# Optimization experiments

Measured on AMD Instinct MI355X. Metric: run time of the kernel, lower is better.

Reference implementation:

```python
import jax, jax.numpy as jnp
import numpy as np

B, P, D, G, N_IMGS, TEMP = 16, 4096, 512, 64, 5000, 0.01


def bilinear_grid_sample(img, grid):
    """F.grid_sample(img, grid, mode='bilinear', padding_mode='zeros', align_corners=False).
    img: (B, C, H, W); grid: (B, Hg, Wg, 2) with grid[...,0]=x, grid[...,1]=y in [-1,1].
    Returns (B, C, Hg*Wg)."""
    b, c, h, w = img.shape
    gx = grid[..., 0].reshape(b, -1)  # (B, N)
    gy = grid[..., 1].reshape(b, -1)
    # align_corners=False mapping to pixel coords
    ix = ((gx + 1.0) * w - 1.0) * 0.5
    iy = ((gy + 1.0) * h - 1.0) * 0.5
    ix0 = jnp.floor(ix)
    iy0 = jnp.floor(iy)
    ix1 = ix0 + 1.0
    iy1 = iy0 + 1.0
    wx1 = ix - ix0
    wx0 = 1.0 - wx1
    wy1 = iy - iy0
    wy0 = 1.0 - wy1
    flat = img.reshape(b, c, h * w)

    def gather(xi, yi):
        valid = (xi >= 0) & (xi < w) & (yi >= 0) & (yi < h)
        idx = (jnp.clip(yi, 0, h - 1) * w + jnp.clip(xi, 0, w - 1)).astype(jnp.int32)
        vals = jnp.take_along_axis(flat, jnp.broadcast_to(idx[:, None, :], (b, c, idx.shape[-1])), axis=2)
        return vals * valid[:, None, :].astype(img.dtype)

    out = (gather(ix0, iy0) * (wx0 * wy0)[:, None, :]
           + gather(ix1, iy0) * (wx1 * wy0)[:, None, :]
           + gather(ix0, iy1) * (wx0 * wy1)[:, None, :]
           + gather(ix1, iy1) * (wx1 * wy1)[:, None, :])
    return out  # (B, C, N)


def setup_inputs() -> dict:
    key = jax.random.key(0)
    ks = jax.random.split(key, 12)
    sc = 1.0 / np.sqrt(D)
    return {
        "x": jax.random.normal(ks[0], (B, P, D), dtype=jnp.float32),
        "Wq": jax.random.normal(ks[1], (D, D), dtype=jnp.float32) * sc,
        "bq": jnp.zeros((D,), dtype=jnp.float32),
        "Wk": jax.random.normal(ks[2], (D, D), dtype=jnp.float32) * sc,
        "bk": jnp.zeros((D,), dtype=jnp.float32),
        "Wv": jax.random.normal(ks[3], (D, D), dtype=jnp.float32) * sc,
        "bv": jnp.zeros((D,), dtype=jnp.float32),
        "avgs": jnp.zeros((N_IMGS, 2, P), dtype=jnp.float32),
        "std_devs": jnp.ones((N_IMGS, 2, P), dtype=jnp.float32),
        "noise_x": jax.random.normal(ks[4], (B, 1, P), dtype=jnp.float32),
        "noise_y": jax.random.normal(ks[5], (B, 1, P), dtype=jnp.float32),
        "img_ids": jax.random.randint(ks[6], (B,), 0, N_IMGS),
        "mask": jnp.ones((B, P), dtype=bool),
    }


def reference(x, Wq, bq, Wk, bk, Wv, bv, avgs, std_devs, noise_x, noise_y, img_ids, mask):
    b, s, d = x.shape
    q = x @ Wq.T + bq
    k = x @ Wk.T + bk
    v = x @ Wv.T + bv
    a = avgs[img_ids]       # (B, 2, P)
    sd = std_devs[img_ids]  # (B, 2, P)
    sample_x = jnp.tanh((noise_x + a[:, 0:1, :]) * sd[:, 0:1, :])  # (B,1,P)
    sample_y = jnp.tanh((noise_y + a[:, 1:2, :]) * sd[:, 1:2, :])  # (B,1,P)
    grid = jnp.concatenate([sample_x, sample_y], axis=1).reshape(b, G, G, 2)
    k_img = jnp.transpose(k, (0, 2, 1)).reshape(b, d, G, G)
    v_img = jnp.transpose(v, (0, 2, 1)).reshape(b, d, G, G)
    sampled_k = jnp.transpose(bilinear_grid_sample(k_img, grid), (0, 2, 1))  # (B, P, D)
    sampled_v = jnp.transpose(bilinear_grid_sample(v_img, grid), (0, 2, 1))
    scores = jnp.sum(sampled_k * q, axis=-1)  # (B, P)
    attention = jax.nn.sigmoid(TEMP * scores)[..., None] * sampled_v  # (B, P, D)
    return attention
```

## Files before the change

kernel.cpp:

```cpp
#include <hip/hip_runtime.h>
#include <math.h>


typedef __attribute__((ext_vector_type(8))) short s16x8;
typedef __attribute__((ext_vector_type(4))) float f32x4;

__device__ __forceinline__ unsigned short f2bf(float f) {
    unsigned u = __float_as_uint(f);
    u += 0x7FFFu + ((u >> 16) & 1u);
    return (unsigned short)(u >> 16);
}

__device__ __forceinline__ void gload_lds16(const void* g, void* l) {
    __builtin_amdgcn_global_load_lds(
        (const __attribute__((address_space(1))) unsigned int*)g,
        (__attribute__((address_space(3))) unsigned int*)l, 16, 0, 0);
}

__global__ __launch_bounds__(256) void cvt_all(
    const float* __restrict__ x, const float* __restrict__ Wq,
    const float* __restrict__ Wk, const float* __restrict__ Wv,
    unsigned short* __restrict__ xbf, unsigned short* __restrict__ wbf)
{
    const int i = blockIdx.x * 256 + threadIdx.x;
    const float* src;
    unsigned short* dst;
    size_t off;
    if (i < 4194304) {
        src = x; dst = xbf; off = (size_t)i;
    } else {
        int t = i - 4194304;
        int w = t >> 15;
        off = (size_t)(t & 32767);
        src = (w == 0) ? Wq : (w == 1 ? Wk : Wv);
        dst = wbf + (size_t)w * 512 * 512;
    }
    const float4* s = (const float4*)src + 2 * off;
    float4 a = s[0], b = s[1];
    uint4 o;
    o.x = (unsigned)f2bf(a.x) | ((unsigned)f2bf(a.y) << 16);
    o.y = (unsigned)f2bf(a.z) | ((unsigned)f2bf(a.w) << 16);
    o.z = (unsigned)f2bf(b.x) | ((unsigned)f2bf(b.y) << 16);
    o.w = (unsigned)f2bf(b.z) | ((unsigned)f2bf(b.w) << 16);
    ((uint4*)dst)[off] = o;
}

template<int T, int NVM, bool STAGE>
__device__ __forceinline__ void tile_step(
    char* ldsc, const unsigned short* aP, const unsigned short* bP,
    int tid, int abase, int bbase, f32x4 (&acc)[8][4])
{
    asm volatile("s_waitcnt vmcnt(%0)" :: "i"(NVM) : "memory");
    __builtin_amdgcn_s_barrier();
    __builtin_amdgcn_sched_barrier(0);
    const char* lp = ldsc + (T & 3) * 32768;
    s16x8 bfr[4], af[4];
    #pragma unroll
    for (int j = 0; j < 4; ++j) bfr[j] = *(const s16x8*)(lp + bbase + j * 256);
    #pragma unroll
    for (int u = 0; u < 4; ++u) af[u] = *(const s16x8*)(lp + abase + u * 256);
    if (STAGE) {
        const int bo = ((T + 3) & 3) * 32768;
        gload_lds16(aP + (T + 3) * 32,      ldsc + bo + tid * 16);
        gload_lds16(aP + (T + 3) * 32 + 16, ldsc + bo + 8192 + tid * 16);
    }
    __builtin_amdgcn_s_barrier();
    asm volatile("s_waitcnt lgkmcnt(0)");
    __builtin_amdgcn_sched_barrier(0);
    __builtin_amdgcn_s_setprio(1);
    #pragma unroll
    for (int u = 0; u < 4; ++u)
        #pragma unroll
        for (int j = 0; j < 4; ++j)
            acc[u][j] = __builtin_amdgcn_mfma_f32_16x16x32_bf16(
                bfr[j], af[u], acc[u][j], 0, 0, 0);
    __builtin_amdgcn_s_setprio(0);
    __builtin_amdgcn_s_barrier();
    __builtin_amdgcn_sched_barrier(0);
    #pragma unroll
    for (int u = 0; u < 4; ++u)
        af[u] = *(const s16x8*)(lp + abase + 1024 + u * 256);
    if (STAGE) {
        const int bo = ((T + 3) & 3) * 32768;
        gload_lds16(bP + (T + 3) * 32,      ldsc + bo + 16384 + tid * 16);
        gload_lds16(bP + (T + 3) * 32 + 16, ldsc + bo + 24576 + tid * 16);
    }
    __builtin_amdgcn_s_barrier();
    asm volatile("s_waitcnt lgkmcnt(0)");
    __builtin_amdgcn_sched_barrier(0);
    __builtin_amdgcn_s_setprio(1);
    #pragma unroll
    for (int u = 0; u < 4; ++u)
        #pragma unroll
        for (int j = 0; j < 4; ++j)
            acc[4 + u][j] = __builtin_amdgcn_mfma_f32_16x16x32_bf16(
                bfr[j], af[u], acc[4 + u][j], 0, 0, 0);
    __builtin_amdgcn_s_setprio(0);
}

__global__ __launch_bounds__(512, 1) void qkv_gemm(
    const unsigned short* __restrict__ xbf,
    const unsigned short* __restrict__ wbf,
    const float* __restrict__ bq, const float* __restrict__ bk,
    const float* __restrict__ bv,
    float* __restrict__ qout,
    unsigned short* __restrict__ kbf,
    unsigned short* __restrict__ vbf)
{
    __shared__ __align__(16) short lds[4][16384];

    const int tid  = threadIdx.x;
    const int lane = tid & 63, wid = tid >> 6;
    const int wr = wid >> 2, wc = wid & 3;

    const int bid = blockIdx.x;
    const int wgid = (bid & 7) * 192 + (bid >> 3);
    const int mt = wgid / 6, nt = wgid % 6;
    const int m0 = mt * 256, n0 = nt * 256;

    const int srow = tid & 255;
    const unsigned short* aP = xbf + (size_t)(m0 + srow) * 512 + (tid >> 8) * 8;
    const unsigned short* bP = wbf + (size_t)(n0 + srow) * 512 + (tid >> 8) * 8;
    char* ldsc = (char*)lds;

    f32x4 acc[8][4] = {};

    const int abase = (lane >> 4) * 4096 + (wr * 128 + (lane & 15)) * 16;
    const int bbase = 16384 + (lane >> 4) * 4096 + (wc * 64 + (lane & 15)) * 16;

    #pragma unroll
    for (int t = 0; t < 3; ++t) {
        const int bo = t * 32768;
        gload_lds16(aP + t * 32,      ldsc + bo + tid * 16);
        gload_lds16(aP + t * 32 + 16, ldsc + bo + 8192 + tid * 16);
        gload_lds16(bP + t * 32,      ldsc + bo + 16384 + tid * 16);
        gload_lds16(bP + t * 32 + 16, ldsc + bo + 24576 + tid * 16);
    }

    tile_step< 0, 8, true >(ldsc, aP, bP, tid, abase, bbase, acc);
    tile_step< 1, 8, true >(ldsc, aP, bP, tid, abase, bbase, acc);
    tile_step< 2, 8, true >(ldsc, aP, bP, tid, abase, bbase, acc);
    tile_step< 3, 8, true >(ldsc, aP, bP, tid, abase, bbase, acc);
    tile_step< 4, 8, true >(ldsc, aP, bP, tid, abase, bbase, acc);
    tile_step< 5, 8, true >(ldsc, aP, bP, tid, abase, bbase, acc);
    tile_step< 6, 8, true >(ldsc, aP, bP, tid, abase, bbase, acc);
    tile_step< 7, 8, true >(ldsc, aP, bP, tid, abase, bbase, acc);
    tile_step< 8, 8, true >(ldsc, aP, bP, tid, abase, bbase, acc);
    tile_step< 9, 8, true >(ldsc, aP, bP, tid, abase, bbase, acc);
    tile_step<10, 8, true >(ldsc, aP, bP, tid, abase, bbase, acc);
    tile_step<11, 8, true >(ldsc, aP, bP, tid, abase, bbase, acc);
    tile_step<12, 8, true >(ldsc, aP, bP, tid, abase, bbase, acc);
    tile_step<13, 8, false>(ldsc, aP, bP, tid, abase, bbase, acc);
    tile_step<14, 4, false>(ldsc, aP, bP, tid, abase, bbase, acc);
    tile_step<15, 0, false>(ldsc, aP, bP, tid, abase, bbase, acc);

    const int sel = nt >> 1;
    const float* bias = sel == 0 ? bq : (sel == 1 ? bk : bv);
    const int rowg = m0 + wr * 128 + (lane & 15);
    const int colg = (n0 & 511) + wc * 64 + (lane >> 4) * 4;

    if (sel == 0) {
        #pragma unroll
        for (int j = 0; j < 4; ++j) {
            const float4 b4 = *(const float4*)&bias[colg + j * 16];
            #pragma unroll
            for (int i = 0; i < 8; ++i) {
                float4 o;
                o.x = acc[i][j][0] + b4.x; o.y = acc[i][j][1] + b4.y;
                o.z = acc[i][j][2] + b4.z; o.w = acc[i][j][3] + b4.w;
                *(float4*)&qout[(size_t)(rowg + i * 16) * 512 + colg + j * 16] = o;
            }
        }
    } else {
        unsigned short* dst = (sel == 1) ? kbf : vbf;
        #pragma unroll
        for (int j = 0; j < 4; ++j) {
            const float4 b4 = *(const float4*)&bias[colg + j * 16];
            #pragma unroll
            for (int i = 0; i < 8; ++i) {
                uint2 o;
                o.x = (unsigned)f2bf(acc[i][j][0] + b4.x)
                    | ((unsigned)f2bf(acc[i][j][1] + b4.y) << 16);
                o.y = (unsigned)f2bf(acc[i][j][2] + b4.z)
                    | ((unsigned)f2bf(acc[i][j][3] + b4.w) << 16);
                *(uint2*)&dst[(size_t)(rowg + i * 16) * 512 + colg + j * 16] = o;
            }
        }
    }
}

__global__ __launch_bounds__(256) void sample_attn(
    float* __restrict__ qo,
    const unsigned short* __restrict__ kbf,
    const unsigned short* __restrict__ vbf,
    const float* __restrict__ avgs,
    const float* __restrict__ stds,
    const float* __restrict__ nx,
    const float* __restrict__ ny,
    const int* __restrict__ img_ids)
{
    const int lane = threadIdx.x & 63;
    const int wid  = threadIdx.x >> 6;
    const int point = (blockIdx.x << 2) + wid;
    const int b = point >> 12;
    const int n = point & 4095;
    const int g1 = n >> 6, g2 = n & 63;
    const int f0 = g1 * 128 + g2 * 2;
    const int id = img_ids[b];

    float g[2];
    #pragma unroll
    for (int c = 0; c < 2; ++c) {
        int f = f0 + c;
        int ch = f >> 12;
        int p  = f & 4095;
        float noise = ch ? ny[(size_t)b * 4096 + p] : nx[(size_t)b * 4096 + p];
        size_t o = ((size_t)id * 2 + ch) * 4096 + p;
        g[c] = tanhf((noise + avgs[o]) * stds[o]);
    }

    float ix = (g[0] + 1.0f) * 32.0f - 0.5f;
    float iy = (g[1] + 1.0f) * 32.0f - 0.5f;
    float fx0 = floorf(ix), fy0 = floorf(iy);
    float wx1 = ix - fx0, wx0 = 1.0f - wx1;
    float wy1 = iy - fy0, wy0 = 1.0f - wy1;
    int x0 = (int)fx0, y0 = (int)fy0;
    int x1 = x0 + 1, y1 = y0 + 1;
    bool vx0 = (x0 >= 0) & (x0 < 64), vx1 = (x1 >= 0) & (x1 < 64);
    bool vy0 = (y0 >= 0) & (y0 < 64), vy1 = (y1 >= 0) & (y1 < 64);
    float w00 = (vx0 & vy0) ? wx0 * wy0 : 0.0f;
    float w10 = (vx1 & vy0) ? wx1 * wy0 : 0.0f;
    float w01 = (vx0 & vy1) ? wx0 * wy1 : 0.0f;
    float w11 = (vx1 & vy1) ? wx1 * wy1 : 0.0f;
    int cx0 = min(max(x0, 0), 63), cx1 = min(max(x1, 0), 63);
    int cy0 = min(max(y0, 0), 63), cy1 = min(max(y1, 0), 63);

    const size_t base = (size_t)b * 4096 * 512;
    const size_t r00 = base + (size_t)(cy0 * 64 + cx0) * 512;
    const size_t r10 = base + (size_t)(cy0 * 64 + cx1) * 512;
    const size_t r01 = base + (size_t)(cy1 * 64 + cx0) * 512;
    const size_t r11 = base + (size_t)(cy1 * 64 + cx1) * 512;

    float* qrow = qo + base + (size_t)n * 512;
    const int c = lane * 8;

    float4 q0 = *(const float4*)(qrow + c);
    float4 q1 = *(const float4*)(qrow + c + 4);

    float sk[8], sv[8];
    {
        uint4 u00k = *(const uint4*)(kbf + r00 + c);
        uint4 u10k = *(const uint4*)(kbf + r10 + c);
        uint4 u01k = *(const uint4*)(kbf + r01 + c);
        uint4 u11k = *(const uint4*)(kbf + r11 + c);
        uint4 u00v = *(const uint4*)(vbf + r00 + c);
        uint4 u10v = *(const uint4*)(vbf + r10 + c);
        uint4 u01v = *(const uint4*)(vbf + r01 + c);
        uint4 u11v = *(const uint4*)(vbf + r11 + c);
        const unsigned* p00k = (const unsigned*)&u00k;
        const unsigned* p10k = (const unsigned*)&u10k;
        const unsigned* p01k = (const unsigned*)&u01k;
        const unsigned* p11k = (const unsigned*)&u11k;
        const unsigned* p00v = (const unsigned*)&u00v;
        const unsigned* p10v = (const unsigned*)&u10v;
        const unsigned* p01v = (const unsigned*)&u01v;
        const unsigned* p11v = (const unsigned*)&u11v;
        #pragma unroll
        for (int t = 0; t < 4; ++t) {
            float a00 = __uint_as_float(p00k[t] << 16);
            float b00 = __uint_as_float(p00k[t] & 0xFFFF0000u);
            float a10 = __uint_as_float(p10k[t] << 16);
            float b10 = __uint_as_float(p10k[t] & 0xFFFF0000u);
            float a01 = __uint_as_float(p01k[t] << 16);
            float b01 = __uint_as_float(p01k[t] & 0xFFFF0000u);
            float a11 = __uint_as_float(p11k[t] << 16);
            float b11 = __uint_as_float(p11k[t] & 0xFFFF0000u);
            sk[2 * t]     = w00 * a00 + w10 * a10 + w01 * a01 + w11 * a11;
            sk[2 * t + 1] = w00 * b00 + w10 * b10 + w01 * b01 + w11 * b11;
            a00 = __uint_as_float(p00v[t] << 16);
            b00 = __uint_as_float(p00v[t] & 0xFFFF0000u);
            a10 = __uint_as_float(p10v[t] << 16);
            b10 = __uint_as_float(p10v[t] & 0xFFFF0000u);
            a01 = __uint_as_float(p01v[t] << 16);
            b01 = __uint_as_float(p01v[t] & 0xFFFF0000u);
            a11 = __uint_as_float(p11v[t] << 16);
            b11 = __uint_as_float(p11v[t] & 0xFFFF0000u);
            sv[2 * t]     = w00 * a00 + w10 * a10 + w01 * a01 + w11 * a11;
            sv[2 * t + 1] = w00 * b00 + w10 * b10 + w01 * b01 + w11 * b11;
        }
    }

    const float qv[8] = {q0.x, q0.y, q0.z, q0.w, q1.x, q1.y, q1.z, q1.w};
    float score = 0.0f;
    #pragma unroll
    for (int t = 0; t < 8; ++t) score += qv[t] * sk[t];
    #pragma unroll
    for (int off = 32; off > 0; off >>= 1)
        score += __shfl_xor(score, off);

    const float sig = 1.0f / (1.0f + expf(-0.01f * score));
    float4 oA, oB;
    oA.x = sig * sv[0]; oA.y = sig * sv[1]; oA.z = sig * sv[2]; oA.w = sig * sv[3];
    oB.x = sig * sv[4]; oB.y = sig * sv[5]; oB.z = sig * sv[6]; oB.w = sig * sv[7];
    *(float4*)(qrow + c) = oA;
    *(float4*)(qrow + c + 4) = oB;
}

extern "C" void kernel_launch(void* const* d_in, const int* in_sizes, int n_in,
                              void* d_out, int out_size, void* d_ws, size_t ws_size,
                              hipStream_t stream)
{
    const float* x    = (const float*)d_in[0];
    const float* Wq   = (const float*)d_in[1];
    const float* bq   = (const float*)d_in[2];
    const float* Wk   = (const float*)d_in[3];
    const float* bk   = (const float*)d_in[4];
    const float* Wv   = (const float*)d_in[5];
    const float* bv   = (const float*)d_in[6];
    const float* avgs = (const float*)d_in[7];
    const float* stds = (const float*)d_in[8];
    const float* nx   = (const float*)d_in[9];
    const float* ny   = (const float*)d_in[10];
    const int* img_ids = (const int*)d_in[11];

    float* out = (float*)d_out;

    unsigned short* xbf = (unsigned short*)d_ws;
    unsigned short* wbf = xbf + (size_t)65536 * 512;
    unsigned short* kbf = wbf + (size_t)1536 * 512;
    unsigned short* vbf = kbf + (size_t)65536 * 512;

    cvt_all<<<16768, 256, 0, stream>>>(x, Wq, Wk, Wv, xbf, wbf);

    qkv_gemm<<<1536, 512, 0, stream>>>(xbf, wbf, bq, bk, bv, out, kbf, vbf);

    sample_attn<<<16384, 256, 0, stream>>>(out, kbf, vbf, avgs, stds, nx, ny, img_ids);
}
```

Baseline: 319.8 us.

## Store Q as bf16 in output buffer and stage GEMM epilogue through LDS

The GEMM epilogue now writes all three projections (Q, K, V) as bf16, packed into a swizzled LDS tile and then written out with coalesced 16-byte row stores. Q is stored as bf16 with a 1024-element row stride inside the fp32 output buffer, so each row occupies the first half of the space its fp32 output row will later use. The sampling kernel reads Q as bf16 and writes fp32 results in place. This halves Q write and read traffic and improves store coalescing, at the cost of extra LDS round-trips and barriers, and Q loses precision from bf16 rounding.

New measurement: 294.0 us. 8.1% less time.

```diff
diff --git a/kernel.cpp b/kernel.cpp
--- a/kernel.cpp
+++ b/kernel.cpp
@@ -103,7 +103,7 @@
     const unsigned short* __restrict__ wbf,
     const float* __restrict__ bq, const float* __restrict__ bk,
     const float* __restrict__ bv,
-    float* __restrict__ qout,
+    unsigned short* __restrict__ qbf,
     unsigned short* __restrict__ kbf,
     unsigned short* __restrict__ vbf)
 {
@@ -156,35 +156,39 @@
 
     const int sel = nt >> 1;
     const float* bias = sel == 0 ? bq : (sel == 1 ? bk : bv);
-    const int rowg = m0 + wr * 128 + (lane & 15);
-    const int colg = (n0 & 511) + wc * 64 + (lane >> 4) * 4;
-
-    if (sel == 0) {
-        #pragma unroll
-        for (int j = 0; j < 4; ++j) {
-            const float4 b4 = *(const float4*)&bias[colg + j * 16];
-            #pragma unroll
-            for (int i = 0; i < 8; ++i) {
-                float4 o;
-                o.x = acc[i][j][0] + b4.x; o.y = acc[i][j][1] + b4.y;
-                o.z = acc[i][j][2] + b4.z; o.w = acc[i][j][3] + b4.w;
-                *(float4*)&qout[(size_t)(rowg + i * 16) * 512 + colg + j * 16] = o;
-            }
+    const int rowl = wr * 128 + (lane & 15);
+    const int coll = wc * 64 + ((lane >> 4) << 2);
+    const int colg = (n0 & 511) + coll;
+
+    __syncthreads();
+    #pragma unroll
+    for (int j = 0; j < 4; ++j) {
+        const float4 b4 = *(const float4*)&bias[colg + j * 16];
+        #pragma unroll
+        for (int i = 0; i < 8; ++i) {
+            const int row = rowl + i * 16;
+            const int cb  = (coll + j * 16) * 2;
+            const int byt = row * 512 + (((cb & ~15) ^ ((row & 7) << 4)) | (cb & 15));
+            uint2 o;
+            o.x = (unsigned)f2bf(acc[i][j][0] + b4.x)
+                | ((unsigned)f2bf(acc[i][j][1] + b4.y) << 16);
+            o.y = (unsigned)f2bf(acc[i][j][2] + b4.z)
+                | ((unsigned)f2bf(acc[i][j][3] + b4.w) << 16);
+            *(uint2*)(ldsc + byt) = o;
         }
-    } else {
-        unsigned short* dst = (sel == 1) ? kbf : vbf;
-        #pragma unroll
-        for (int j = 0; j < 4; ++j) {
-            const float4 b4 = *(const float4*)&bias[colg + j * 16];
-            #pragma unroll
-            for (int i = 0; i < 8; ++i) {
-                uint2 o;
-                o.x = (unsigned)f2bf(acc[i][j][0] + b4.x)
-                    | ((unsigned)f2bf(acc[i][j][1] + b4.y) << 16);
-                o.y = (unsigned)f2bf(acc[i][j][2] + b4.z)
-                    | ((unsigned)f2bf(acc[i][j][3] + b4.w) << 16);
-                *(uint2*)&dst[(size_t)(rowg + i * 16) * 512 + colg + j * 16] = o;
-            }
+    }
+    __syncthreads();
+    {
+        unsigned short* dst = (sel == 0) ? qbf : (sel == 1 ? kbf : vbf);
+        const size_t rstride = (sel == 0) ? 1024 : 512;
+        const int rr = tid >> 5;
+        const int cc = tid & 31;
+        #pragma unroll
+        for (int s = 0; s < 16; ++s) {
+            const int r = s * 16 + rr;
+            const int byt = r * 512 + ((cc * 16) ^ ((r & 7) << 4));
+            uint4 d = *(const uint4*)(ldsc + byt);
+            *(uint4*)&dst[(size_t)(m0 + r) * rstride + (n0 & 511) + cc * 8] = d;
         }
     }
 }
@@ -241,11 +245,20 @@
     const size_t r01 = base + (size_t)(cy1 * 64 + cx0) * 512;
     const size_t r11 = base + (size_t)(cy1 * 64 + cx1) * 512;
 
-    float* qrow = qo + base + (size_t)n * 512;
     const int c = lane * 8;
 
-    float4 q0 = *(const float4*)(qrow + c);
-    float4 q1 = *(const float4*)(qrow + c + 4);
+    const unsigned short* qrowb =
+        (const unsigned short*)qo + ((size_t)(b * 4096 + n)) * 1024;
+    uint4 qu = *(const uint4*)(qrowb + c);
+    float qv[8];
+    {
+        const unsigned* qp = (const unsigned*)&qu;
+        #pragma unroll
+        for (int t = 0; t < 4; ++t) {
+            qv[2 * t]     = __uint_as_float(qp[t] << 16);
+            qv[2 * t + 1] = __uint_as_float(qp[t] & 0xFFFF0000u);
+        }
+    }
 
     float sk[8], sv[8];
     {
@@ -290,7 +303,6 @@
         }
     }
 
-    const float qv[8] = {q0.x, q0.y, q0.z, q0.w, q1.x, q1.y, q1.z, q1.w};
     float score = 0.0f;
     #pragma unroll
     for (int t = 0; t < 8; ++t) score += qv[t] * sk[t];
@@ -299,11 +311,12 @@
         score += __shfl_xor(score, off);
 
     const float sig = 1.0f / (1.0f + expf(-0.01f * score));
+    float* orow = qo + ((size_t)(b * 4096 + n)) * 512;
     float4 oA, oB;
     oA.x = sig * sv[0]; oA.y = sig * sv[1]; oA.z = sig * sv[2]; oA.w = sig * sv[3];
     oB.x = sig * sv[4]; oB.y = sig * sv[5]; oB.z = sig * sv[6]; oB.w = sig * sv[7];
-    *(float4*)(qrow + c) = oA;
-    *(float4*)(qrow + c + 4) = oB;
+    *(float4*)(orow + c) = oA;
+    *(float4*)(orow + c + 4) = oB;
 }
 
 extern "C" void kernel_launch(void* const* d_in, const int* in_sizes, int n_in,
@@ -332,7 +345,8 @@
 
     cvt_all<<<16768, 256, 0, stream>>>(x, Wq, Wk, Wv, xbf, wbf);
 
-    qkv_gemm<<<1536, 512, 0, stream>>>(xbf, wbf, bq, bk, bv, out, kbf, vbf);
+    qkv_gemm<<<1536, 512, 0, stream>>>(xbf, wbf, bq, bk, bv,
+                                       (unsigned short*)d_out, kbf, vbf);
 
     sample_attn<<<16384, 256, 0, stream>>>(out, kbf, vbf, avgs, stds, nx, ny, img_ids);
 }
```
